# Optimization experiments

Hardware: AMD Instinct MI355X
Metric: run time of the kernel (lower is better)

Reference implementation:

```python
import jax, jax.numpy as jnp
import numpy as np

N, E, D = 50000, 800000, 256

def setup_inputs() -> dict:
    key = jax.random.key(0)
    ks = jax.random.split(key, 12)
    s = 1.0 / np.sqrt(D)
    return {
        "x": jax.random.normal(ks[0], (N, D), dtype=jnp.float32),
        "src": jax.random.randint(ks[1], (E,), 0, N, dtype=jnp.int64),
        "dst": jax.random.randint(ks[2], (E,), 0, N, dtype=jnp.int64),
        "W_w": jax.random.normal(ks[3], (D, D), dtype=jnp.float32) * s,
        "W_b": jnp.zeros((D,), dtype=jnp.float32),
        "U_w": jax.random.normal(ks[4], (D, D), dtype=jnp.float32) * s,
        "U_b": jnp.zeros((D,), dtype=jnp.float32),
        "V_w": jax.random.normal(ks[5], (D, D), dtype=jnp.float32) * s,
        "V_b": jnp.zeros((D,), dtype=jnp.float32),
        "attn_l": jax.random.normal(ks[6], (D,), dtype=jnp.float32) * s,
        "attn_r": jax.random.normal(ks[7], (D,), dtype=jnp.float32) * s,
        "gamma": jnp.ones((D,), dtype=jnp.float32),
        "beta": jnp.zeros((D,), dtype=jnp.float32),
    }

def reference(x, src, dst, W_w, W_b, U_w, U_b, V_w, V_b, attn_l, attn_r, gamma, beta):
    # node transforms (dropout p=0 -> identity)
    Wh = x @ W_w + W_b            # [N, D]
    Uh = x @ U_w + U_b            # [N, D]
    Vh = x @ V_w + V_b            # [N, D]
    out_src = Wh * attn_l         # [N, D]
    out_dst = Wh * attn_r         # [N, D]
    # per-edge gate: sigma = sigmoid(out_src[u] + out_dst[v])  [E, D]
    sigma = jax.nn.sigmoid(out_src[src] + out_dst[dst])
    # aggregate to destination nodes
    sum_sigma_h = jax.ops.segment_sum(Vh[src] * sigma, dst, num_segments=N)
    sum_sigma = jax.ops.segment_sum(sigma, dst, num_segments=N)
    h = Uh + sum_sigma_h / (sum_sigma + 1e-6)
    # layer norm (eps=1e-6, affine)
    mu = jnp.mean(h, axis=-1, keepdims=True)
    var = jnp.mean((h - mu) ** 2, axis=-1, keepdims=True)
    h = (h - mu) / jnp.sqrt(var + 1e-6) * gamma + beta
    h = jax.nn.relu(h)
    return x + h  # residual
```

## Files before the change

kernel.cpp:

```cpp
#include <hip/hip_runtime.h>
#include <hip/hip_bf16.h>

#define NN 50000
#define NE 800000
#define NB 196

typedef __attribute__((ext_vector_type(8))) short short8;
typedef __attribute__((ext_vector_type(4))) float floatx4;
typedef unsigned short u16;
typedef unsigned int u32;

__device__ __forceinline__ u16 f2bf(float f) {
    u32 u = __float_as_uint(f);
    u += 0x7FFFu + ((u >> 16) & 1u);
    return (u16)(u >> 16);
}
__device__ __forceinline__ float bf_lo(u32 u) { return __uint_as_float(u << 16); }
__device__ __forceinline__ float bf_hi(u32 u) { return __uint_as_float(u & 0xFFFF0000u); }
__device__ __forceinline__ u32 pack_bf(float lo, float hi) {
    return (u32)f2bf(lo) | ((u32)f2bf(hi) << 16);
}
__device__ __forceinline__ void gl_lds16(const void* g, void* l) {
    __builtin_amdgcn_global_load_lds((const __attribute__((address_space(1))) void*)g,
                                     (__attribute__((address_space(3))) void*)l, 16, 0, 0);
}

__global__ __launch_bounds__(256) void tw_kernel(const float* __restrict__ W, const float* __restrict__ U,
                                                 const float* __restrict__ V, u16* __restrict__ wT) {
    __shared__ float s[32][33];
    int g = blockIdx.z;
    const float* M = (g == 0) ? W : ((g == 1) ? U : V);
    int r0 = blockIdx.x * 32, c0 = blockIdx.y * 32;
    int tx = threadIdx.x & 31, ty = threadIdx.x >> 5;
#pragma unroll
    for (int k = 0; k < 4; ++k)
        s[ty + k * 8][tx] = M[(size_t)(r0 + ty + k * 8) * 256 + c0 + tx];
    __syncthreads();
#pragma unroll
    for (int k = 0; k < 4; ++k)
        wT[(size_t)(g * 256 + c0 + ty + k * 8) * 256 + r0 + tx] = f2bf(s[tx][ty + k * 8]);
}

__global__ void hist_kernel(const int* __restrict__ dst, int* __restrict__ deg) {
    int e = blockIdx.x * 256 + threadIdx.x;
    if (e < NE) atomicAdd(&deg[dst[e]], 1);
}

__global__ __launch_bounds__(256) void scanA_kernel(const int* __restrict__ deg, int* __restrict__ bsum) {
    int t = threadIdx.x;
    int i = blockIdx.x * 256 + t;
    int v = (i < NN) ? deg[i] : 0;
#pragma unroll
    for (int m = 32; m; m >>= 1) v += __shfl_xor(v, m, 64);
    __shared__ int ws[4];
    if ((t & 63) == 0) ws[t >> 6] = v;
    __syncthreads();
    if (t == 0) bsum[blockIdx.x] = ws[0] + ws[1] + ws[2] + ws[3];
}

__global__ __launch_bounds__(256) void scanB_kernel(const int* __restrict__ bsum, int* __restrict__ bpre,
                                                    int* __restrict__ rows_end) {
    int t = threadIdx.x, lane = t & 63, wv = t >> 6;
    int v = (t < NB) ? bsum[t] : 0;
    int inc = v;
#pragma unroll
    for (int off = 1; off < 64; off <<= 1) {
        int u = __shfl_up(inc, off, 64);
        if (lane >= off) inc += u;
    }
    __shared__ int wsum[4];
    if (lane == 63) wsum[wv] = inc;
    __syncthreads();
    int woff = 0;
    for (int k = 0; k < wv; ++k) woff += wsum[k];
    if (t < NB) bpre[t] = woff + inc - v;
    if (t == 255) rows_end[0] = woff + inc;
}

__global__ __launch_bounds__(256) void scanC_kernel(const int* __restrict__ deg, const int* __restrict__ bpre,
                                                    int* __restrict__ rows, int* __restrict__ cursor) {
    int t = threadIdx.x, lane = t & 63, wv = t >> 6;
    int i = blockIdx.x * 256 + t;
    int v = (i < NN) ? deg[i] : 0;
    int inc = v;
#pragma unroll
    for (int off = 1; off < 64; off <<= 1) {
        int u = __shfl_up(inc, off, 64);
        if (lane >= off) inc += u;
    }
    __shared__ int wsum[4];
    if (lane == 63) wsum[wv] = inc;
    __syncthreads();
    int woff = bpre[blockIdx.x];
    for (int k = 0; k < wv; ++k) woff += wsum[k];
    int excl = woff + inc - v;
    if (i < NN) { rows[i] = excl; cursor[i] = excl; }
}

__global__ void scatter_kernel(const int* __restrict__ src, const int* __restrict__ dst,
                               int* __restrict__ cursor, int* __restrict__ esrc) {
    int e = blockIdx.x * 256 + threadIdx.x;
    if (e < NE) {
        int d = dst[e];
        int pos = atomicAdd(&cursor[d], 1);
        esrc[pos] = src[e];
    }
}

__global__ __launch_bounds__(256) void gemm_kernel(
    const float* __restrict__ x, const u16* __restrict__ wT,
    const float* __restrict__ Wb, const float* __restrict__ Ub, const float* __restrict__ Vb,
    u16* __restrict__ WVh, float* __restrict__ Uh) {
    __shared__ __align__(16) u16 As[128 * 64];
    __shared__ __align__(16) u16 Bs[128 * 64];

    int rb = blockIdx.x * 128;
    int cbg = blockIdx.y * 128;
    int t = threadIdx.x, lane = t & 63, w = t >> 6;
    int wm = w >> 1, wn = w & 1;

    floatx4 acc[4][4] = {};

    int b_subrow = lane >> 3;
    int b_q = lane & 7;
    int a_row = t >> 1;
    int a_half = t & 1;

    for (int kt = 0; kt < 4; ++kt) {
        int k0 = kt * 64;
#pragma unroll
        for (int ii = 0; ii < 4; ++ii) {
            int rowbase = (w * 4 + ii) * 8;
            int row = rowbase + b_subrow;
            int qa = b_q ^ (row & 7);
            gl_lds16(wT + (size_t)(cbg + row) * 256 + k0 + qa * 8, Bs + rowbase * 64);
        }
        int grow = rb + a_row;
        uint4 pk[4] = {};
        if (grow < NN) {
            const float* px = x + (size_t)grow * 256 + k0 + a_half * 32;
#pragma unroll
            for (int c = 0; c < 4; ++c) {
                floatx4 f0 = *(const floatx4*)(px + c * 8);
                floatx4 f1 = *(const floatx4*)(px + c * 8 + 4);
                pk[c].x = pack_bf(f0[0], f0[1]);
                pk[c].y = pack_bf(f0[2], f0[3]);
                pk[c].z = pack_bf(f1[0], f1[1]);
                pk[c].w = pack_bf(f1[2], f1[3]);
            }
        }
#pragma unroll
        for (int c = 0; c < 4; ++c) {
            int q = a_half * 4 + c;
            *(uint4*)(As + a_row * 64 + ((q ^ (a_row & 7)) * 8)) = pk[c];
        }
        __syncthreads();

#pragma unroll
        for (int s = 0; s < 2; ++s) {
            short8 a[4], b[4];
#pragma unroll
            for (int i = 0; i < 4; ++i) {
                int ar = wm * 64 + i * 16 + (lane & 15);
                int q = s * 4 + (lane >> 4);
                a[i] = *(const short8*)(As + ar * 64 + ((q ^ (ar & 7)) * 8));
                int br = wn * 64 + i * 16 + (lane & 15);
                b[i] = *(const short8*)(Bs + br * 64 + ((q ^ (br & 7)) * 8));
            }
#pragma unroll
            for (int i = 0; i < 4; ++i)
#pragma unroll
                for (int j = 0; j < 4; ++j)
                    acc[i][j] = __builtin_amdgcn_mfma_f32_16x16x32_bf16(a[i], b[j], acc[i][j], 0, 0, 0);
        }
        __syncthreads();
    }

    int g = cbg >> 8;
    int cloc = cbg & 255;
    const float* bias = (g == 0) ? Wb : ((g == 1) ? Ub : Vb);
#pragma unroll
    for (int i = 0; i < 4; ++i)
#pragma unroll
        for (int j = 0; j < 4; ++j) {
            int col = cloc + wn * 64 + j * 16 + (lane & 15);
            float bv = bias[col];
#pragma unroll
            for (int r = 0; r < 4; ++r) {
                int row = rb + wm * 64 + i * 16 + (lane >> 4) * 4 + r;
                if (row < NN) {
                    float val = acc[i][j][r] + bv;
                    if (g == 0)      WVh[(size_t)row * 512 + col] = f2bf(val);
                    else if (g == 1) Uh[(size_t)row * 256 + col] = val;
                    else             WVh[(size_t)row * 512 + 256 + col] = f2bf(val);
                }
            }
        }
}

__global__ __launch_bounds__(256) void node_kernel(
    const u16* __restrict__ WVh, const float* __restrict__ x,
    const int* __restrict__ rows, const int* __restrict__ esrc,
    const float* __restrict__ attn_l, const float* __restrict__ attn_r,
    const float* __restrict__ gamma, const float* __restrict__ beta,
    float* inout) {
    int wv = threadIdx.x >> 6, lane = threadIdx.x & 63;
    int v = blockIdx.x * 4 + wv;
    if (v >= NN) return;
    int c0 = lane * 4;

    floatx4 al = *(const floatx4*)(attn_l + c0);
    floatx4 ar = *(const floatx4*)(attn_r + c0);

    uint2 wvv = *(const uint2*)(WVh + (size_t)v * 512 + c0);
    float td[4] = { bf_lo(wvv.x) * ar[0], bf_hi(wvv.x) * ar[1],
                    bf_lo(wvv.y) * ar[2], bf_hi(wvv.y) * ar[3] };

    float acc_h[4] = {0.f, 0.f, 0.f, 0.f};
    float acc_s[4] = {0.f, 0.f, 0.f, 0.f};

    int e0 = rows[v], e1 = rows[v + 1];
    for (int e = e0; e < e1; ++e) {
        int u = esrc[e];
        const u16* base = WVh + (size_t)u * 512 + c0;
        uint2 wu = *(const uint2*)(base);
        uint2 vu = *(const uint2*)(base + 256);
        float wf[4] = { bf_lo(wu.x), bf_hi(wu.x), bf_lo(wu.y), bf_hi(wu.y) };
        float vf[4] = { bf_lo(vu.x), bf_hi(vu.x), bf_lo(vu.y), bf_hi(vu.y) };
#pragma unroll
        for (int j = 0; j < 4; ++j) {
            float tt = fmaf(wf[j], al[j], td[j]);
            float s = __builtin_amdgcn_rcpf(1.0f + __expf(-tt));
            acc_s[j] += s;
            acc_h[j] = fmaf(s, vf[j], acc_h[j]);
        }
    }

    floatx4 uh = *(const floatx4*)(inout + (size_t)v * 256 + c0);
    float h[4];
#pragma unroll
    for (int j = 0; j < 4; ++j)
        h[j] = uh[j] + acc_h[j] * __builtin_amdgcn_rcpf(acc_s[j] + 1e-6f);

    float s01 = h[0] + h[1] + h[2] + h[3];
#pragma unroll
    for (int m = 32; m; m >>= 1) s01 += __shfl_xor(s01, m, 64);
    float mu = s01 * (1.0f / 256.0f);
    float d[4] = { h[0] - mu, h[1] - mu, h[2] - mu, h[3] - mu };
    float sq = d[0] * d[0] + d[1] * d[1] + d[2] * d[2] + d[3] * d[3];
#pragma unroll
    for (int m = 32; m; m >>= 1) sq += __shfl_xor(sq, m, 64);
    float inv = rsqrtf(sq * (1.0f / 256.0f) + 1e-6f);

    floatx4 gm = *(const floatx4*)(gamma + c0);
    floatx4 bt = *(const floatx4*)(beta + c0);
    floatx4 xr = *(const floatx4*)(x + (size_t)v * 256 + c0);
    floatx4 res;
#pragma unroll
    for (int j = 0; j < 4; ++j) {
        float y = d[j] * inv * gm[j] + bt[j];
        y = fmaxf(y, 0.0f);
        res[j] = xr[j] + y;
    }
    *(floatx4*)(inout + (size_t)v * 256 + c0) = res;
}

extern "C" void kernel_launch(void* const* d_in, const int* in_sizes, int n_in,
                              void* d_out, int out_size, void* d_ws, size_t ws_size,
                              hipStream_t stream) {
    const float* x       = (const float*)d_in[0];
    const int*   src     = (const int*)d_in[1];
    const int*   dst     = (const int*)d_in[2];
    const float* W_w     = (const float*)d_in[3];
    const float* W_b     = (const float*)d_in[4];
    const float* U_w     = (const float*)d_in[5];
    const float* U_b     = (const float*)d_in[6];
    const float* V_w     = (const float*)d_in[7];
    const float* V_b     = (const float*)d_in[8];
    const float* attn_l  = (const float*)d_in[9];
    const float* attn_r  = (const float*)d_in[10];
    const float* gamma   = (const float*)d_in[11];
    const float* beta    = (const float*)d_in[12];

    char* ws = (char*)d_ws;
    size_t off = 0;
    auto alloc = [&](size_t bytes) -> char* {
        char* p = ws + off;
        off += (bytes + 255) & ~(size_t)255;
        return p;
    };
    u16* WVh     = (u16*)alloc((size_t)NN * 512 * 2);
    u16* wT      = (u16*)alloc((size_t)768 * 256 * 2);
    int* deg     = (int*)alloc((size_t)NN * 4);
    int* rows    = (int*)alloc((size_t)(NN + 1) * 4);
    int* cursor  = (int*)alloc((size_t)NN * 4);
    int* esrc    = (int*)alloc((size_t)NE * 4);
    int* bsum    = (int*)alloc((size_t)NB * 4);
    int* bpre    = (int*)alloc((size_t)NB * 4);

    float* Uh_f32 = (float*)d_out;

    hipMemsetAsync(deg, 0, (size_t)NN * 4, stream);

    tw_kernel<<<dim3(8, 8, 3), 256, 0, stream>>>(W_w, U_w, V_w, wT);
    hist_kernel<<<(NE + 255) / 256, 256, 0, stream>>>(dst, deg);
    scanA_kernel<<<NB, 256, 0, stream>>>(deg, bsum);
    scanB_kernel<<<1, 256, 0, stream>>>(bsum, bpre, rows + NN);
    scanC_kernel<<<NB, 256, 0, stream>>>(deg, bpre, rows, cursor);
    scatter_kernel<<<(NE + 255) / 256, 256, 0, stream>>>(src, dst, cursor, esrc);

    dim3 gg((NN + 127) / 128, 6);
    gemm_kernel<<<gg, 256, 0, stream>>>(x, wT, W_b, U_b, V_b, WVh, Uh_f32);

    node_kernel<<<(NN + 3) / 4, 256, 0, stream>>>(
        WVh, x, rows, esrc, attn_l, attn_r, gamma, beta, (float*)d_out);
}
```

Measured before the change: 339.3 us.

## Fuse prep and scatter into combined launches, prestage bf16 x, widen GEMM tiles, batch edge loads

Merges the weight transpose, degree histogram and a new x→bf16 conversion into one prep launch. The CSR scatter is folded into the GEMM launch as extra blocks. The GEMM now loads pre-converted bf16 x directly into LDS via global_load_lds and computes 256-column tiles per block, halving A reloads. The node kernel batches 8 edge gathers at a time for memory-level parallelism and uses exp2 with prescaled coefficients. The extra x conversion pass adds about 75 MB of traffic, and the bf16 path depends on workspace size.

```diff
diff --git a/kernel.cpp b/kernel.cpp
--- a/kernel.cpp
+++ b/kernel.cpp
@@ -4,6 +4,13 @@
 #define NN 50000
 #define NE 800000
 #define NB 196
+#define NROWPAD 50048
+
+#define XCVT_BLOCKS 6250
+#define TW_BLOCKS   192
+#define HIST_BLOCKS 3125
+#define SCAT_BLOCKS 3125
+#define GEMM_BLOCKS (391*3)
 
 typedef __attribute__((ext_vector_type(8))) short short8;
 typedef __attribute__((ext_vector_type(4))) float floatx4;
@@ -25,25 +32,45 @@
                                      (__attribute__((address_space(3))) void*)l, 16, 0, 0);
 }
 
-__global__ __launch_bounds__(256) void tw_kernel(const float* __restrict__ W, const float* __restrict__ U,
-                                                 const float* __restrict__ V, u16* __restrict__ wT) {
+#if __has_builtin(__builtin_amdgcn_exp2f)
+#define EXP2F(x) __builtin_amdgcn_exp2f(x)
+#else
+#define EXP2F(x) exp2f(x)
+#endif
+
+__global__ __launch_bounds__(256) void prep_kernel(
+    const float* __restrict__ x, u16* __restrict__ xbf,
+    const float* __restrict__ W, const float* __restrict__ U, const float* __restrict__ V,
+    u16* __restrict__ wT, const int* __restrict__ dst, int* __restrict__ deg) {
     __shared__ float s[32][33];
-    int g = blockIdx.z;
-    const float* M = (g == 0) ? W : ((g == 1) ? U : V);
-    int r0 = blockIdx.x * 32, c0 = blockIdx.y * 32;
-    int tx = threadIdx.x & 31, ty = threadIdx.x >> 5;
-#pragma unroll
-    for (int k = 0; k < 4; ++k)
-        s[ty + k * 8][tx] = M[(size_t)(r0 + ty + k * 8) * 256 + c0 + tx];
-    __syncthreads();
-#pragma unroll
-    for (int k = 0; k < 4; ++k)
-        wT[(size_t)(g * 256 + c0 + ty + k * 8) * 256 + r0 + tx] = f2bf(s[tx][ty + k * 8]);
-}
-
-__global__ void hist_kernel(const int* __restrict__ dst, int* __restrict__ deg) {
-    int e = blockIdx.x * 256 + threadIdx.x;
-    if (e < NE) atomicAdd(&deg[dst[e]], 1);
+    int b = blockIdx.x;
+    if (b < XCVT_BLOCKS) {
+        size_t i = ((size_t)b * 256 + threadIdx.x) * 8;
+        floatx4 f0 = *(const floatx4*)(x + i);
+        floatx4 f1 = *(const floatx4*)(x + i + 4);
+        uint4 pk;
+        pk.x = pack_bf(f0[0], f0[1]);
+        pk.y = pack_bf(f0[2], f0[3]);
+        pk.z = pack_bf(f1[0], f1[1]);
+        pk.w = pack_bf(f1[2], f1[3]);
+        *(uint4*)(xbf + i) = pk;
+    } else if (b < XCVT_BLOCKS + TW_BLOCKS) {
+        int bb = b - XCVT_BLOCKS;
+        int g = bb >> 6, rem = bb & 63;
+        int r0 = (rem & 7) * 32, c0 = (rem >> 3) * 32;
+        const float* M = (g == 0) ? W : ((g == 1) ? U : V);
+        int tx = threadIdx.x & 31, ty = threadIdx.x >> 5;
+#pragma unroll
+        for (int k = 0; k < 4; ++k)
+            s[ty + k * 8][tx] = M[(size_t)(r0 + ty + k * 8) * 256 + c0 + tx];
+        __syncthreads();
+#pragma unroll
+        for (int k = 0; k < 4; ++k)
+            wT[(size_t)(g * 256 + c0 + ty + k * 8) * 256 + r0 + tx] = f2bf(s[tx][ty + k * 8]);
+    } else {
+        int e = (b - XCVT_BLOCKS - TW_BLOCKS) * 256 + threadIdx.x;
+        if (e < NE) atomicAdd(&deg[dst[e]], 1);
+    }
 }
 
 __global__ __launch_bounds__(256) void scanA_kernel(const int* __restrict__ deg, int* __restrict__ bsum) {
@@ -97,32 +124,38 @@
     if (i < NN) { rows[i] = excl; cursor[i] = excl; }
 }
 
-__global__ void scatter_kernel(const int* __restrict__ src, const int* __restrict__ dst,
-                               int* __restrict__ cursor, int* __restrict__ esrc) {
-    int e = blockIdx.x * 256 + threadIdx.x;
-    if (e < NE) {
-        int d = dst[e];
-        int pos = atomicAdd(&cursor[d], 1);
-        esrc[pos] = src[e];
-    }
-}
-
-__global__ __launch_bounds__(256) void gemm_kernel(
-    const float* __restrict__ x, const u16* __restrict__ wT,
+template<bool USE_BF>
+__global__ __launch_bounds__(256, 2) void gemmsc_kernel(
+    const u16* __restrict__ xbf, const float* __restrict__ xf, const u16* __restrict__ wT,
     const float* __restrict__ Wb, const float* __restrict__ Ub, const float* __restrict__ Vb,
-    u16* __restrict__ WVh, float* __restrict__ Uh) {
+    u16* __restrict__ WVh, float* __restrict__ Uh,
+    const int* __restrict__ src, const int* __restrict__ dst,
+    int* __restrict__ cursor, int* __restrict__ esrc) {
     __shared__ __align__(16) u16 As[128 * 64];
-    __shared__ __align__(16) u16 Bs[128 * 64];
-
-    int rb = blockIdx.x * 128;
-    int cbg = blockIdx.y * 128;
+    __shared__ __align__(16) u16 Bs[2][128 * 64];
+
+    int b = blockIdx.x;
+    if (b < SCAT_BLOCKS) {
+        int e = b * 256 + threadIdx.x;
+        if (e < NE) {
+            int d = dst[e];
+            int pos = atomicAdd(&cursor[d], 1);
+            esrc[pos] = src[e];
+        }
+        return;
+    }
+    int gb = b - SCAT_BLOCKS;
+    int rb = (gb % 391) * 128;
+    int cgy = gb / 391;
+    int cbg = cgy * 256;
+
     int t = threadIdx.x, lane = t & 63, w = t >> 6;
     int wm = w >> 1, wn = w & 1;
 
-    floatx4 acc[4][4] = {};
-
-    int b_subrow = lane >> 3;
-    int b_q = lane & 7;
+    floatx4 acc[2][4][4] = {};
+
+    int subrow = lane >> 3;
+    int qv = lane & 7;
     int a_row = t >> 1;
     int a_half = t & 1;
 
@@ -131,71 +164,84 @@
 #pragma unroll
         for (int ii = 0; ii < 4; ++ii) {
             int rowbase = (w * 4 + ii) * 8;
-            int row = rowbase + b_subrow;
-            int qa = b_q ^ (row & 7);
-            gl_lds16(wT + (size_t)(cbg + row) * 256 + k0 + qa * 8, Bs + rowbase * 64);
-        }
-        int grow = rb + a_row;
-        uint4 pk[4] = {};
-        if (grow < NN) {
-            const float* px = x + (size_t)grow * 256 + k0 + a_half * 32;
+            int row = rowbase + subrow;
+            int qa = qv ^ (row & 7);
+            gl_lds16(wT + (size_t)(cbg + row) * 256 + k0 + qa * 8, Bs[0] + rowbase * 64);
+            gl_lds16(wT + (size_t)(cbg + 128 + row) * 256 + k0 + qa * 8, Bs[1] + rowbase * 64);
+            if (USE_BF)
+                gl_lds16(xbf + (size_t)(rb + row) * 256 + k0 + qa * 8, As + rowbase * 64);
+        }
+        if (!USE_BF) {
+            int grow = rb + a_row;
+            uint4 pk[4] = {};
+            if (grow < NN) {
+                const float* px = xf + (size_t)grow * 256 + k0 + a_half * 32;
+#pragma unroll
+                for (int c = 0; c < 4; ++c) {
+                    floatx4 f0 = *(const floatx4*)(px + c * 8);
+                    floatx4 f1 = *(const floatx4*)(px + c * 8 + 4);
+                    pk[c].x = pack_bf(f0[0], f0[1]);
+                    pk[c].y = pack_bf(f0[2], f0[3]);
+                    pk[c].z = pack_bf(f1[0], f1[1]);
+                    pk[c].w = pack_bf(f1[2], f1[3]);
+                }
+            }
 #pragma unroll
             for (int c = 0; c < 4; ++c) {
-                floatx4 f0 = *(const floatx4*)(px + c * 8);
-                floatx4 f1 = *(const floatx4*)(px + c * 8 + 4);
-                pk[c].x = pack_bf(f0[0], f0[1]);
-                pk[c].y = pack_bf(f0[2], f0[3]);
-                pk[c].z = pack_bf(f1[0], f1[1]);
-                pk[c].w = pack_bf(f1[2], f1[3]);
+                int q = a_half * 4 + c;
+                *(uint4*)(As + a_row * 64 + ((q ^ (a_row & 7)) * 8)) = pk[c];
             }
         }
-#pragma unroll
-        for (int c = 0; c < 4; ++c) {
-            int q = a_half * 4 + c;
-            *(uint4*)(As + a_row * 64 + ((q ^ (a_row & 7)) * 8)) = pk[c];
-        }
         __syncthreads();
 
 #pragma unroll
         for (int s = 0; s < 2; ++s) {
-            short8 a[4], b[4];
+            short8 a[4], bfr[2][4];
+            int q = s * 4 + (lane >> 4);
 #pragma unroll
             for (int i = 0; i < 4; ++i) {
                 int ar = wm * 64 + i * 16 + (lane & 15);
-                int q = s * 4 + (lane >> 4);
                 a[i] = *(const short8*)(As + ar * 64 + ((q ^ (ar & 7)) * 8));
-                int br = wn * 64 + i * 16 + (lane & 15);
-                b[i] = *(const short8*)(Bs + br * 64 + ((q ^ (br & 7)) * 8));
             }
 #pragma unroll
-            for (int i = 0; i < 4; ++i)
-#pragma unroll
-                for (int j = 0; j < 4; ++j)
-                    acc[i][j] = __builtin_amdgcn_mfma_f32_16x16x32_bf16(a[i], b[j], acc[i][j], 0, 0, 0);
+            for (int ch = 0; ch < 2; ++ch)
+#pragma unroll
+                for (int j = 0; j < 4; ++j) {
+                    int br = wn * 64 + j * 16 + (lane & 15);
+                    bfr[ch][j] = *(const short8*)(Bs[ch] + br * 64 + ((q ^ (br & 7)) * 8));
+                }
+#pragma unroll
+            for (int ch = 0; ch < 2; ++ch)
+#pragma unroll
+                for (int i = 0; i < 4; ++i)
+#pragma unroll
+                    for (int j = 0; j < 4; ++j)
+                        acc[ch][i][j] = __builtin_amdgcn_mfma_f32_16x16x32_bf16(
+                            a[i], bfr[ch][j], acc[ch][i][j], 0, 0, 0);
         }
         __syncthreads();
     }
 
-    int g = cbg >> 8;
-    int cloc = cbg & 255;
-    const float* bias = (g == 0) ? Wb : ((g == 1) ? Ub : Vb);
-#pragma unroll
-    for (int i = 0; i < 4; ++i)
-#pragma unroll
-        for (int j = 0; j < 4; ++j) {
-            int col = cloc + wn * 64 + j * 16 + (lane & 15);
-            float bv = bias[col];
-#pragma unroll
-            for (int r = 0; r < 4; ++r) {
-                int row = rb + wm * 64 + i * 16 + (lane >> 4) * 4 + r;
-                if (row < NN) {
-                    float val = acc[i][j][r] + bv;
-                    if (g == 0)      WVh[(size_t)row * 512 + col] = f2bf(val);
-                    else if (g == 1) Uh[(size_t)row * 256 + col] = val;
-                    else             WVh[(size_t)row * 512 + 256 + col] = f2bf(val);
+    const float* bias = (cgy == 0) ? Wb : ((cgy == 1) ? Ub : Vb);
+#pragma unroll
+    for (int ch = 0; ch < 2; ++ch)
+#pragma unroll
+        for (int i = 0; i < 4; ++i)
+#pragma unroll
+            for (int j = 0; j < 4; ++j) {
+                int col = ch * 128 + wn * 64 + j * 16 + (lane & 15);
+                float bv = bias[col];
+#pragma unroll
+                for (int r = 0; r < 4; ++r) {
+                    int row = rb + wm * 64 + i * 16 + (lane >> 4) * 4 + r;
+                    if (row < NN) {
+                        float val = acc[ch][i][j][r] + bv;
+                        if (cgy == 0)      WVh[(size_t)row * 512 + col] = f2bf(val);
+                        else if (cgy == 1) Uh[(size_t)row * 256 + col] = val;
+                        else               WVh[(size_t)row * 512 + 256 + col] = f2bf(val);
+                    }
                 }
             }
-        }
 }
 
 __global__ __launch_bounds__(256) void node_kernel(
@@ -209,31 +255,57 @@
     if (v >= NN) return;
     int c0 = lane * 4;
 
-    floatx4 al = *(const floatx4*)(attn_l + c0);
-    floatx4 ar = *(const floatx4*)(attn_r + c0);
-
+    const float NL2E = -1.44269504f;
+    floatx4 alv = *(const floatx4*)(attn_l + c0);
+    floatx4 arv = *(const floatx4*)(attn_r + c0);
     uint2 wvv = *(const uint2*)(WVh + (size_t)v * 512 + c0);
-    float td[4] = { bf_lo(wvv.x) * ar[0], bf_hi(wvv.x) * ar[1],
-                    bf_lo(wvv.y) * ar[2], bf_hi(wvv.y) * ar[3] };
+    float al2[4] = { alv[0] * NL2E, alv[1] * NL2E, alv[2] * NL2E, alv[3] * NL2E };
+    float td2[4] = { bf_lo(wvv.x) * arv[0] * NL2E, bf_hi(wvv.x) * arv[1] * NL2E,
+                     bf_lo(wvv.y) * arv[2] * NL2E, bf_hi(wvv.y) * arv[3] * NL2E };
 
     float acc_h[4] = {0.f, 0.f, 0.f, 0.f};
     float acc_s[4] = {0.f, 0.f, 0.f, 0.f};
 
-    int e0 = rows[v], e1 = rows[v + 1];
-    for (int e = e0; e < e1; ++e) {
-        int u = esrc[e];
-        const u16* base = WVh + (size_t)u * 512 + c0;
-        uint2 wu = *(const uint2*)(base);
-        uint2 vu = *(const uint2*)(base + 256);
+    auto edge = [&](uint2 wu, uint2 vu) {
         float wf[4] = { bf_lo(wu.x), bf_hi(wu.x), bf_lo(wu.y), bf_hi(wu.y) };
         float vf[4] = { bf_lo(vu.x), bf_hi(vu.x), bf_lo(vu.y), bf_hi(vu.y) };
 #pragma unroll
         for (int j = 0; j < 4; ++j) {
-            float tt = fmaf(wf[j], al[j], td[j]);
-            float s = __builtin_amdgcn_rcpf(1.0f + __expf(-tt));
+            float m = fmaf(wf[j], al2[j], td2[j]);
+            float s = __builtin_amdgcn_rcpf(1.0f + EXP2F(m));
             acc_s[j] += s;
             acc_h[j] = fmaf(s, vf[j], acc_h[j]);
         }
+    };
+
+    int e = rows[v], e1 = rows[v + 1];
+    for (; e + 8 <= e1; e += 8) {
+        int us[8];
+#pragma unroll
+        for (int q = 0; q < 8; ++q) us[q] = esrc[e + q];
+        uint2 wu[8], vu[8];
+#pragma unroll
+        for (int q = 0; q < 8; ++q) {
+            const u16* p = WVh + (size_t)us[q] * 512 + c0;
+            wu[q] = *(const uint2*)p;
+            vu[q] = *(const uint2*)(p + 256);
+        }
+#pragma unroll
+        for (int q = 0; q < 8; ++q) edge(wu[q], vu[q]);
+    }
+    for (; e + 2 <= e1; e += 2) {
+        int ua = esrc[e], ub = esrc[e + 1];
+        const u16* pa = WVh + (size_t)ua * 512 + c0;
+        const u16* pb = WVh + (size_t)ub * 512 + c0;
+        uint2 wa = *(const uint2*)pa, va = *(const uint2*)(pa + 256);
+        uint2 wb = *(const uint2*)pb, vb = *(const uint2*)(pb + 256);
+        edge(wa, va); edge(wb, vb);
+    }
+    for (; e < e1; ++e) {
+        int u = esrc[e];
+        const u16* p = WVh + (size_t)u * 512 + c0;
+        uint2 wu = *(const uint2*)p, vu = *(const uint2*)(p + 256);
+        edge(wu, vu);
     }
 
     floatx4 uh = *(const floatx4*)(inout + (size_t)v * 256 + c0);
@@ -297,20 +369,33 @@
     int* esrc    = (int*)alloc((size_t)NE * 4);
     int* bsum    = (int*)alloc((size_t)NB * 4);
     int* bpre    = (int*)alloc((size_t)NB * 4);
+    u16* xbf     = (u16*)alloc((size_t)NROWPAD * 256 * 2);
+    bool use_bf  = (ws_size >= off);
 
     float* Uh_f32 = (float*)d_out;
 
     hipMemsetAsync(deg, 0, (size_t)NN * 4, stream);
 
-    tw_kernel<<<dim3(8, 8, 3), 256, 0, stream>>>(W_w, U_w, V_w, wT);
-    hist_kernel<<<(NE + 255) / 256, 256, 0, stream>>>(dst, deg);
+    if (use_bf) {
+        prep_kernel<<<XCVT_BLOCKS + TW_BLOCKS + HIST_BLOCKS, 256, 0, stream>>>(
+            x, xbf, W_w, U_w, V_w, wT, dst, deg);
+    } else {
+        prep_kernel<<<XCVT_BLOCKS + TW_BLOCKS + HIST_BLOCKS, 256, 0, stream>>>(
+            x, (u16*)wT , W_w, U_w, V_w, wT, dst, deg);
+    }
+
     scanA_kernel<<<NB, 256, 0, stream>>>(deg, bsum);
     scanB_kernel<<<1, 256, 0, stream>>>(bsum, bpre, rows + NN);
     scanC_kernel<<<NB, 256, 0, stream>>>(deg, bpre, rows, cursor);
-    scatter_kernel<<<(NE + 255) / 256, 256, 0, stream>>>(src, dst, cursor, esrc);
-
-    dim3 gg((NN + 127) / 128, 6);
-    gemm_kernel<<<gg, 256, 0, stream>>>(x, wT, W_b, U_b, V_b, WVh, Uh_f32);
+
+    int gs_blocks = SCAT_BLOCKS + GEMM_BLOCKS;
+    if (use_bf) {
+        gemmsc_kernel<true><<<gs_blocks, 256, 0, stream>>>(
+            xbf, x, wT, W_b, U_b, V_b, WVh, Uh_f32, src, dst, cursor, esrc);
+    } else {
+        gemmsc_kernel<false><<<gs_blocks, 256, 0, stream>>>(
+            nullptr, x, wT, W_b, U_b, V_b, WVh, Uh_f32, src, dst, cursor, esrc);
+    }
 
     node_kernel<<<(NN + 3) / 4, 256, 0, stream>>>(
         WVh, x, rows, esrc, attn_l, attn_r, gamma, beta, (float*)d_out);
```

Result: faster. 295.4 us (-12.9%).
